# Optimization experiments

Hardware: AMD Instinct MI355X
Metric: run time of the kernel (lower is better)

The kernel has to match this reference:

```python
import jax, jax.numpy as jnp
import numpy as np

B, T, IN, H, OUT = 128, 1024, 17, 512, 17


def setup_inputs() -> dict:
    key = jax.random.key(0)
    ks = jax.random.split(key, 11)
    s_in = 1.0 / np.sqrt(H)
    return {
        "x": jax.random.normal(ks[0], (B, T, IN), dtype=jnp.float32),
        "wih0": jax.random.normal(ks[1], (4 * H, IN), dtype=jnp.float32) * s_in,
        "whh0": jax.random.normal(ks[2], (4 * H, H), dtype=jnp.float32) * s_in,
        "bih0": jax.random.normal(ks[3], (4 * H,), dtype=jnp.float32) * s_in,
        "bhh0": jax.random.normal(ks[4], (4 * H,), dtype=jnp.float32) * s_in,
        "wih1": jax.random.normal(ks[5], (4 * H, H), dtype=jnp.float32) * s_in,
        "whh1": jax.random.normal(ks[6], (4 * H, H), dtype=jnp.float32) * s_in,
        "bih1": jax.random.normal(ks[7], (4 * H,), dtype=jnp.float32) * s_in,
        "bhh1": jax.random.normal(ks[8], (4 * H,), dtype=jnp.float32) * s_in,
        "lin_w": jax.random.normal(ks[9], (OUT, H), dtype=jnp.float32) * s_in,
        "lin_b": jax.random.normal(ks[10], (OUT,), dtype=jnp.float32) * s_in,
    }


def _lstm_layer(x, wih, whh, bih, bhh):
    # x: [B, T, D]; gate order i, f, g, o (torch.nn.LSTMCell convention)
    b, _, _ = x.shape
    h = whh.shape[1]
    # Precompute input projection for all timesteps: [B, T, 4H]
    proj = jnp.einsum("btd,gd->btg", x, wih) + bih

    def step(carry, p_t):
        h_t, c_t = carry
        gates = p_t + h_t @ whh.T + bhh  # [B, 4H]
        i, f, g, o = jnp.split(gates, 4, axis=1)
        i = jax.nn.sigmoid(i)
        f = jax.nn.sigmoid(f)
        o = jax.nn.sigmoid(o)
        g = jnp.tanh(g)
        c_t = f * c_t + i * g
        h_t = o * jnp.tanh(c_t)
        return (h_t, c_t), h_t

    h0 = jnp.zeros((b, h), x.dtype)
    c0 = jnp.zeros((b, h), x.dtype)
    _, ys = jax.lax.scan(step, (h0, c0), jnp.swapaxes(proj, 0, 1))  # ys: [T, B, H]
    return jnp.swapaxes(ys, 0, 1)  # [B, T, H]


def reference(x, wih0, whh0, bih0, bhh0, wih1, whh1, bih1, bhh1, lin_w, lin_b):
    y = _lstm_layer(x, wih0, whh0, bih0, bhh0)
    y = _lstm_layer(y, wih1, whh1, bih1, bhh1)
    h_last = y[:, -1, :]  # [B, H]
    return h_last @ lin_w.T + lin_b  # [B, OUT]
```

## Files before the change

### kernel.cpp

```cpp
#include <hip/hip_runtime.h>
#include <cstddef>
#include <cstdint>

typedef unsigned long long ull;
typedef unsigned short u16;
typedef __attribute__((ext_vector_type(8))) short s8v;
typedef __attribute__((ext_vector_type(4))) float f4v;

#define GROUPS 8
#define WPG    32
#define BG     16
#define JS     16
#define TPB    256
#define NT     1024
#define HDIM   512
#define INDIM  17
#define OUTDIM 17
#define BTOT   128
#define RING_D 4

#define AT_LD(p)   __hip_atomic_load((p), __ATOMIC_RELAXED, __HIP_MEMORY_SCOPE_AGENT)
#define AT_ST(p,v) __hip_atomic_store((p), (v), __ATOMIC_RELAXED, __HIP_MEMORY_SCOPE_AGENT)

#define FLAGS_INTS (256 * 16)
#define RING_OFF   ((size_t)FLAGS_INTS * 4)
#define RING_ELEMS ((size_t)RING_D * GROUPS * 2 * BG * HDIM)
#define H1_OFF     (RING_OFF + RING_ELEMS * 2)
#define H1_ELEMS   ((size_t)2 * GROUPS * 2 * BG * HDIM)
#define WS_NEEDED  (H1_OFF + H1_ELEMS * 2)

#define RIDX(sl, gr, pl, b, j) \
  (((((size_t)(sl) * GROUPS + (gr)) * 2 + (pl)) * BG + (b)) * HDIM + (j))
#define H1IDX(pp, gr, pl, b, j) \
  (((((size_t)(pp) * GROUPS + (gr)) * 2 + (pl)) * BG + (b)) * HDIM + (j))

__device__ __forceinline__ u16 f2bf(float f) {
  unsigned int u = __float_as_uint(f);
  u += 0x7FFFu + ((u >> 16) & 1u);
  return (u16)(u >> 16);
}
__device__ __forceinline__ float bf2f(u16 h) {
  return __uint_as_float(((unsigned int)h) << 16);
}
__device__ __forceinline__ float sigm(float x) { return 1.f / (1.f + __expf(-x)); }
__device__ __forceinline__ float tanh_f(float x) { return 2.f / (1.f + __expf(-2.f * x)) - 1.f; }

#define MFMA(a, b, c) __builtin_amdgcn_mfma_f32_16x16x32_bf16((a), (b), (c), 0, 0, 0)

__global__ __launch_bounds__(TPB, 1) void lstm_fused(
    const float* __restrict__ x,
    const float* __restrict__ wih0, const float* __restrict__ whh0,
    const float* __restrict__ bih0, const float* __restrict__ bhh0,
    const float* __restrict__ wih1, const float* __restrict__ whh1,
    const float* __restrict__ bih1, const float* __restrict__ bhh1,
    u16* __restrict__ ring,
    u16* __restrict__ h1b,
    int* __restrict__ flags)
{
  const int bid  = blockIdx.x;
  const int gr   = bid & 7;
  const int wg   = bid >> 3;
  const int j0   = wg * JS;
  const int tid  = threadIdx.x;
  const int wave = tid >> 6;
  const int lane = tid & 63;
  const int n    = lane & 15;
  const int q    = lane >> 4;
  const int k0   = q * 8;

  __shared__ char smem[65536];
  char* b0h = smem;
  char* b0l = smem + 16384;
  char* b1h = smem + 32768;
  char* b1l = smem + 49152;
  float* ldsg = (float*)smem;

  const int row = wave * HDIM + j0 + n;
  s8v w0x_h, w0x_l;
  {
    const float* wr = wih0 + (size_t)row * INDIM;
#pragma unroll
    for (int j = 0; j < 8; ++j) {
      int k = k0 + j;
      float v = (k < INDIM) ? wr[k] : 0.f;
      u16 hi = f2bf(v);
      w0x_h[j] = (short)hi;
      w0x_l[j] = (short)f2bf(v - bf2f(hi));
    }
  }
  s8v w0h_h[16], w0h_l[16];
  {
    const float* wr = whh0 + (size_t)row * HDIM;
#pragma unroll
    for (int kt = 0; kt < 16; ++kt)
#pragma unroll
      for (int j = 0; j < 8; ++j) {
        float v = wr[kt * 32 + k0 + j];
        u16 hi = f2bf(v);
        w0h_h[kt][j] = (short)hi;
        w0h_l[kt][j] = (short)f2bf(v - bf2f(hi));
      }
  }
  s8v w1x_h[16];
  {
    const float* wr = wih1 + (size_t)row * HDIM;
#pragma unroll
    for (int kt = 0; kt < 16; ++kt)
#pragma unroll
      for (int j = 0; j < 8; ++j)
        w1x_h[kt][j] = (short)f2bf(wr[kt * 32 + k0 + j]);
  }
  s8v w1h_h[16], w1h_l[16];
  {
    const float* wr = whh1 + (size_t)row * HDIM;
#pragma unroll
    for (int kt = 0; kt < 16; ++kt)
#pragma unroll
      for (int j = 0; j < 8; ++j) {
        float v = wr[kt * 32 + k0 + j];
        u16 hi = f2bf(v);
        w1h_h[kt][j] = (short)hi;
        w1h_l[kt][j] = (short)f2bf(v - bf2f(hi));
      }
  }
  const float b0v = bih0[row] + bhh0[row];
  const float b1v = bih1[row] + bhh1[row];

  float c0 = 0.f, c1 = 0.f;
  const int b_l = tid >> 4, j_l = tid & 15, jg = j0 + j_l;

  AT_ST(&ring[RIDX(0, gr, 0, b_l, jg)], (u16)0);
  AT_ST(&ring[RIDX(0, gr, 1, b_l, jg)], (u16)0);
  AT_ST(&h1b[H1IDX(0, gr, 0, b_l, jg)], (u16)0);
  AT_ST(&h1b[H1IDX(0, gr, 1, b_l, jg)], (u16)0);
  __syncthreads();
  if (tid == 0) AT_ST(&flags[bid * 16], 1);

  for (int s = 1; s <= NT + 1; ++s) {
    const bool doL0 = (s <= NT);
    const bool doL1 = (s >= 2);

    f4v a0 = {b0v, b0v, b0v, b0v};
    if (doL0) {
      const int t = s - 1;
      const float* xr = x + ((size_t)(gr * BG + n) * NT + t) * INDIM;
      s8v axh, axl;
#pragma unroll
      for (int j = 0; j < 8; ++j) {
        int k = k0 + j;
        float v = (k < INDIM) ? xr[k] : 0.f;
        u16 hi = f2bf(v);
        axh[j] = (short)hi;
        axl[j] = (short)f2bf(v - bf2f(hi));
      }
      a0 = MFMA(axh, w0x_h, a0);
      a0 = MFMA(axl, w0x_h, a0);
      a0 = MFMA(axh, w0x_l, a0);
    }

    if (tid < WPG) {
      const int* fp = &flags[(tid * 8 + gr) * 16];
      while (AT_LD(fp) < s) __builtin_amdgcn_s_sleep(1);
    }
    __syncthreads();

    {
      const int sl  = (s - 1) & (RING_D - 1);
      const int pp1 = s & 1;
      const ull* g0h = (const ull*)(ring + RIDX(sl, gr, 0, 0, 0));
      const ull* g0l = (const ull*)(ring + RIDX(sl, gr, 1, 0, 0));
      const ull* g1h = (const ull*)(h1b + H1IDX(pp1, gr, 0, 0, 0));
      const ull* g1l = (const ull*)(h1b + H1IDX(pp1, gr, 1, 0, 0));
      ull v0h[8], v0l[8], v1h[8], v1l[8];
#pragma unroll
      for (int r = 0; r < 8; ++r) {
        int c = r * 256 + tid;
        v0h[r] = AT_LD(g0h + c);
        v0l[r] = AT_LD(g0l + c);
        v1h[r] = AT_LD(g1h + c);
        v1l[r] = AT_LD(g1l + c);
      }
#pragma unroll
      for (int r = 0; r < 8; ++r) {
        int c = r * 256 + tid;
        int b = c >> 7, k4 = c & 127;
        int off = b * 1024 + ((k4 * 8) ^ ((b & 7) * 16));
        *(ull*)(b0h + off) = v0h[r];
        *(ull*)(b0l + off) = v0l[r];
        *(ull*)(b1h + off) = v1h[r];
        *(ull*)(b1l + off) = v1l[r];
      }
    }
    __syncthreads();

    f4v z = {0.f, 0.f, 0.f, 0.f};
    f4v cA1 = z, cA2 = z, cB0 = {b1v, b1v, b1v, b1v}, cB1 = z;
#pragma unroll
    for (int kt = 0; kt < 16; ++kt) {
      int off = n * 1024 + ((kt * 64 + q * 16) ^ ((n & 7) * 16));
      s8v ah = *(const s8v*)(b0h + off);
      s8v al = *(const s8v*)(b0l + off);
      a0  = MFMA(ah, w0h_h[kt], a0);
      cA1 = MFMA(al, w0h_h[kt], cA1);
      cA2 = MFMA(ah, w0h_l[kt], cA2);
      cB0 = MFMA(ah, w1x_h[kt], cB0);
      cB1 = MFMA(al, w1x_h[kt], cB1);
    }
    f4v cC0 = z, cC1 = z, cC2 = z;
#pragma unroll
    for (int kt = 0; kt < 16; ++kt) {
      int off = n * 1024 + ((kt * 64 + q * 16) ^ ((n & 7) * 16));
      s8v ah = *(const s8v*)(b1h + off);
      s8v al = *(const s8v*)(b1l + off);
      cC0 = MFMA(ah, w1h_h[kt], cC0);
      cC1 = MFMA(al, w1h_h[kt], cC1);
      cC2 = MFMA(ah, w1h_l[kt], cC2);
    }
    __syncthreads();

    if (doL0) {
      f4v g = a0 + cA1 + cA2;
#pragma unroll
      for (int r = 0; r < 4; ++r) ldsg[wave * 256 + (q * 4 + r) * 16 + n] = g[r];
    }
    if (doL1) {
      f4v g = cB0 + cB1 + cC0 + cC1 + cC2;
#pragma unroll
      for (int r = 0; r < 4; ++r) ldsg[(4 + wave) * 256 + (q * 4 + r) * 16 + n] = g[r];
    }
    __syncthreads();

    if (doL0) {
      float pi = ldsg[0 * 256 + tid], pf = ldsg[1 * 256 + tid];
      float pg = ldsg[2 * 256 + tid], po = ldsg[3 * 256 + tid];
      float ig = sigm(pi), fg = sigm(pf), og = sigm(po), gg = tanh_f(pg);
      c0 = fg * c0 + ig * gg;
      float h = og * tanh_f(c0);
      u16 hh = f2bf(h), hl = f2bf(h - bf2f(hh));
      int sl = s & (RING_D - 1);
      AT_ST(&ring[RIDX(sl, gr, 0, b_l, jg)], hh);
      AT_ST(&ring[RIDX(sl, gr, 1, b_l, jg)], hl);
    }
    if (doL1) {
      float pi = ldsg[4 * 256 + tid], pf = ldsg[5 * 256 + tid];
      float pg = ldsg[6 * 256 + tid], po = ldsg[7 * 256 + tid];
      float ig = sigm(pi), fg = sigm(pf), og = sigm(po), gg = tanh_f(pg);
      c1 = fg * c1 + ig * gg;
      float h = og * tanh_f(c1);
      u16 hh = f2bf(h), hl = f2bf(h - bf2f(hh));
      int pw = (s - 1) & 1;
      AT_ST(&h1b[H1IDX(pw, gr, 0, b_l, jg)], hh);
      AT_ST(&h1b[H1IDX(pw, gr, 1, b_l, jg)], hl);
    }
    __syncthreads();
    if (doL0 && tid == 0) AT_ST(&flags[bid * 16], s + 1);
  }
}

__global__ void final_linear(const u16* __restrict__ h1b,
                             const float* __restrict__ lin_w,
                             const float* __restrict__ lin_b,
                             float* __restrict__ out) {
  int b = blockIdx.x, o = threadIdx.x;
  int gr = b >> 4, b_l = b & 15;
  if (o < OUTDIM) {
    float acc = lin_b[o];
    const u16* ph = h1b + H1IDX(0, gr, 0, b_l, 0);
    const u16* pl = h1b + H1IDX(0, gr, 1, b_l, 0);
    for (int j = 0; j < HDIM; ++j) {
      float h = bf2f(ph[j]) + bf2f(pl[j]);
      acc += h * lin_w[(size_t)o * HDIM + j];
    }
    out[b * OUTDIM + o] = acc;
  }
}

__global__ void init_flags(int* __restrict__ flags) {
  int i = blockIdx.x * TPB + threadIdx.x;
  if (i < FLAGS_INTS) flags[i] = 0;
}

__global__ void sentinel_kernel(float* __restrict__ out, int nv) {
  int i = blockIdx.x * TPB + threadIdx.x;
  if (i < nv) out[i] = 1e30f;
}

extern "C" void kernel_launch(void* const* d_in, const int* in_sizes, int n_in,
                              void* d_out, int out_size, void* d_ws, size_t ws_size,
                              hipStream_t stream) {
  const float* x     = (const float*)d_in[0];
  const float* wih0  = (const float*)d_in[1];
  const float* whh0  = (const float*)d_in[2];
  const float* bih0  = (const float*)d_in[3];
  const float* bhh0  = (const float*)d_in[4];
  const float* wih1  = (const float*)d_in[5];
  const float* whh1  = (const float*)d_in[6];
  const float* bih1  = (const float*)d_in[7];
  const float* bhh1  = (const float*)d_in[8];
  const float* lin_w = (const float*)d_in[9];
  const float* lin_b = (const float*)d_in[10];
  float* out = (float*)d_out;
  char* ws = (char*)d_ws;

  if (ws_size < WS_NEEDED) {
    sentinel_kernel<<<(out_size + TPB - 1) / TPB, TPB, 0, stream>>>(out, out_size);
    return;
  }

  int* flags = (int*)ws;
  u16* ring  = (u16*)(ws + RING_OFF);
  u16* h1b   = (u16*)(ws + H1_OFF);

  init_flags<<<(FLAGS_INTS + TPB - 1) / TPB, TPB, 0, stream>>>(flags);
  lstm_fused<<<256, TPB, 0, stream>>>(x, wih0, whh0, bih0, bhh0,
                                      wih1, whh1, bih1, bhh1, ring, h1b, flags);
  final_linear<<<BTOT, 64, 0, stream>>>(h1b, lin_w, lin_b, out);
}
```

Baseline: 5.472 ms.

## Split K across waves and load hidden state directly into MFMA registers

The work split inside each block changes. Before, each wave handled one gate over the full K=512. Now each wave handles all four gates over a 128-wide K slice, and the partial sums are reduced through a swizzled LDS buffer. The hidden-state operands are loaded straight from global memory into MFMA registers, which removes the LDS staging copy and one barrier per step. In exchange, each step adds a cross-wave reduction, and each wave now issues redundant global loads of its own K slice.

```diff
diff --git a/kernel.cpp b/kernel.cpp
--- a/kernel.cpp
+++ b/kernel.cpp
@@ -46,6 +46,13 @@
 __device__ __forceinline__ float tanh_f(float x) { return 2.f / (1.f + __expf(-2.f * x)) - 1.f; }
 
 #define MFMA(a, b, c) __builtin_amdgcn_mfma_f32_16x16x32_bf16((a), (b), (c), 0, 0, 0)
+
+__device__ __forceinline__ s8v ld16(const ull* p) {
+  union { ull q[2]; s8v v; } u;
+  u.q[0] = AT_LD(p);
+  u.q[1] = AT_LD(p + 1);
+  return u.v;
+}
 
 __global__ __launch_bounds__(TPB, 1) void lstm_fused(
     const float* __restrict__ x,
@@ -67,18 +74,13 @@
   const int n    = lane & 15;
   const int q    = lane >> 4;
   const int k0   = q * 8;
-
-  __shared__ char smem[65536];
-  char* b0h = smem;
-  char* b0l = smem + 16384;
-  char* b1h = smem + 32768;
-  char* b1l = smem + 49152;
-  float* ldsg = (float*)smem;
-
-  const int row = wave * HDIM + j0 + n;
+  const int kw   = wave * 128;
+
+  __shared__ float red[4 * 8 * 16 * 16];
+
   s8v w0x_h, w0x_l;
   {
-    const float* wr = wih0 + (size_t)row * INDIM;
+    const float* wr = wih0 + (size_t)(wave * HDIM + j0 + n) * INDIM;
 #pragma unroll
     for (int j = 0; j < 8; ++j) {
       int k = k0 + j;
@@ -88,46 +90,37 @@
       w0x_l[j] = (short)f2bf(v - bf2f(hi));
     }
   }
-  s8v w0h_h[16], w0h_l[16];
-  {
-    const float* wr = whh0 + (size_t)row * HDIM;
-#pragma unroll
-    for (int kt = 0; kt < 16; ++kt)
+  s8v w0hh[4][4], w0hl[4][4], w1xh[4][4], w1hh[4][4], w1hl[4][4];
+#pragma unroll
+  for (int g = 0; g < 4; ++g) {
+    const size_t row = (size_t)(g * HDIM + j0 + n);
+    const float* p0 = whh0 + row * HDIM;
+    const float* p1 = wih1 + row * HDIM;
+    const float* p2 = whh1 + row * HDIM;
+#pragma unroll
+    for (int kt = 0; kt < 4; ++kt) {
 #pragma unroll
       for (int j = 0; j < 8; ++j) {
-        float v = wr[kt * 32 + k0 + j];
-        u16 hi = f2bf(v);
-        w0h_h[kt][j] = (short)hi;
-        w0h_l[kt][j] = (short)f2bf(v - bf2f(hi));
-      }
-  }
-  s8v w1x_h[16];
-  {
-    const float* wr = wih1 + (size_t)row * HDIM;
-#pragma unroll
-    for (int kt = 0; kt < 16; ++kt)
-#pragma unroll
-      for (int j = 0; j < 8; ++j)
-        w1x_h[kt][j] = (short)f2bf(wr[kt * 32 + k0 + j]);
-  }
-  s8v w1h_h[16], w1h_l[16];
-  {
-    const float* wr = whh1 + (size_t)row * HDIM;
-#pragma unroll
-    for (int kt = 0; kt < 16; ++kt)
-#pragma unroll
-      for (int j = 0; j < 8; ++j) {
-        float v = wr[kt * 32 + k0 + j];
-        u16 hi = f2bf(v);
-        w1h_h[kt][j] = (short)hi;
-        w1h_l[kt][j] = (short)f2bf(v - bf2f(hi));
-      }
-  }
-  const float b0v = bih0[row] + bhh0[row];
-  const float b1v = bih1[row] + bhh1[row];
+        int k = kw + kt * 32 + k0 + j;
+        float v0 = p0[k], v2 = p2[k];
+        u16 h0q = f2bf(v0), h2q = f2bf(v2);
+        w0hh[g][kt][j] = (short)h0q;
+        w0hl[g][kt][j] = (short)f2bf(v0 - bf2f(h0q));
+        w1xh[g][kt][j] = (short)f2bf(p1[k]);
+        w1hh[g][kt][j] = (short)h2q;
+        w1hl[g][kt][j] = (short)f2bf(v2 - bf2f(h2q));
+      }
+    }
+  }
+  const int b_l = tid >> 4, j_l = tid & 15, jg = j0 + j_l;
+  float bL0[4], bL1[4];
+#pragma unroll
+  for (int g = 0; g < 4; ++g) {
+    bL0[g] = bih0[g * HDIM + jg] + bhh0[g * HDIM + jg];
+    bL1[g] = bih1[g * HDIM + jg] + bhh1[g * HDIM + jg];
+  }
 
   float c0 = 0.f, c1 = 0.f;
-  const int b_l = tid >> 4, j_l = tid & 15, jg = j0 + j_l;
 
   AT_ST(&ring[RIDX(0, gr, 0, b_l, jg)], (u16)0);
   AT_ST(&ring[RIDX(0, gr, 1, b_l, jg)], (u16)0);
@@ -136,11 +129,13 @@
   __syncthreads();
   if (tid == 0) AT_ST(&flags[bid * 16], 1);
 
+  const f4v z = {0.f, 0.f, 0.f, 0.f};
+
   for (int s = 1; s <= NT + 1; ++s) {
     const bool doL0 = (s <= NT);
     const bool doL1 = (s >= 2);
 
-    f4v a0 = {b0v, b0v, b0v, b0v};
+    f4v xacc = z;
     if (doL0) {
       const int t = s - 1;
       const float* xr = x + ((size_t)(gr * BG + n) * NT + t) * INDIM;
@@ -153,9 +148,9 @@
         axh[j] = (short)hi;
         axl[j] = (short)f2bf(v - bf2f(hi));
       }
-      a0 = MFMA(axh, w0x_h, a0);
-      a0 = MFMA(axl, w0x_h, a0);
-      a0 = MFMA(axh, w0x_l, a0);
+      xacc = MFMA(axh, w0x_h, xacc);
+      xacc = MFMA(axl, w0x_h, xacc);
+      xacc = MFMA(axh, w0x_l, xacc);
     }
 
     if (tid < WPG) {
@@ -164,87 +159,90 @@
     }
     __syncthreads();
 
-    {
-      const int sl  = (s - 1) & (RING_D - 1);
-      const int pp1 = s & 1;
-      const ull* g0h = (const ull*)(ring + RIDX(sl, gr, 0, 0, 0));
-      const ull* g0l = (const ull*)(ring + RIDX(sl, gr, 1, 0, 0));
-      const ull* g1h = (const ull*)(h1b + H1IDX(pp1, gr, 0, 0, 0));
-      const ull* g1l = (const ull*)(h1b + H1IDX(pp1, gr, 1, 0, 0));
-      ull v0h[8], v0l[8], v1h[8], v1l[8];
-#pragma unroll
-      for (int r = 0; r < 8; ++r) {
-        int c = r * 256 + tid;
-        v0h[r] = AT_LD(g0h + c);
-        v0l[r] = AT_LD(g0l + c);
-        v1h[r] = AT_LD(g1h + c);
-        v1l[r] = AT_LD(g1l + c);
-      }
-#pragma unroll
-      for (int r = 0; r < 8; ++r) {
-        int c = r * 256 + tid;
-        int b = c >> 7, k4 = c & 127;
-        int off = b * 1024 + ((k4 * 8) ^ ((b & 7) * 16));
-        *(ull*)(b0h + off) = v0h[r];
-        *(ull*)(b0l + off) = v0l[r];
-        *(ull*)(b1h + off) = v1h[r];
-        *(ull*)(b1l + off) = v1l[r];
-      }
+    const int sl  = (s - 1) & (RING_D - 1);
+    const int pp1 = s & 1;
+    const size_t loff = (size_t)n * HDIM + kw + k0;
+    const ull* r0h = (const ull*)(ring + RIDX(sl, gr, 0, 0, 0) + loff);
+    const ull* r0l = (const ull*)(ring + RIDX(sl, gr, 1, 0, 0) + loff);
+    const ull* r1h = (const ull*)(h1b + H1IDX(pp1, gr, 0, 0, 0) + loff);
+    const ull* r1l = (const ull*)(h1b + H1IDX(pp1, gr, 1, 0, 0) + loff);
+    s8v a0h[4], a0l[4], a1h[4], a1l[4];
+#pragma unroll
+    for (int kt = 0; kt < 4; ++kt) {
+      a0h[kt] = ld16(r0h + kt * 8);
+      a0l[kt] = ld16(r0l + kt * 8);
+    }
+#pragma unroll
+    for (int kt = 0; kt < 4; ++kt) {
+      a1h[kt] = ld16(r1h + kt * 8);
+      a1l[kt] = ld16(r1l + kt * 8);
+    }
+
+    f4v accL0[4] = {z, z, z, z}, accL1[4] = {z, z, z, z};
+#pragma unroll
+    for (int kt = 0; kt < 4; ++kt)
+#pragma unroll
+      for (int g = 0; g < 4; ++g) {
+        accL0[g] = MFMA(a0h[kt], w0hh[g][kt], accL0[g]);
+        accL0[g] = MFMA(a0l[kt], w0hh[g][kt], accL0[g]);
+        accL0[g] = MFMA(a0h[kt], w0hl[g][kt], accL0[g]);
+        accL1[g] = MFMA(a0h[kt], w1xh[g][kt], accL1[g]);
+        accL1[g] = MFMA(a0l[kt], w1xh[g][kt], accL1[g]);
+      }
+#pragma unroll
+    for (int kt = 0; kt < 4; ++kt)
+#pragma unroll
+      for (int g = 0; g < 4; ++g) {
+        accL1[g] = MFMA(a1h[kt], w1hh[g][kt], accL1[g]);
+        accL1[g] = MFMA(a1l[kt], w1hh[g][kt], accL1[g]);
+        accL1[g] = MFMA(a1h[kt], w1hl[g][kt], accL1[g]);
+      }
+    accL0[wave] += xacc;
+
+#pragma unroll
+    for (int lg = 0; lg < 8; ++lg) {
+      const f4v a = (lg < 4) ? accL0[lg] : accL1[lg - 4];
+      int base = ((wave * 8 + lg) * 16 + n) * 16;
+      int idx = (base + ((q * 4) ^ ((n & 3) << 2))) ^ ((n & 4) << 2);
+      *(f4v*)&red[idx] = a;
     }
     __syncthreads();
 
-    f4v z = {0.f, 0.f, 0.f, 0.f};
-    f4v cA1 = z, cA2 = z, cB0 = {b1v, b1v, b1v, b1v}, cB1 = z;
-#pragma unroll
-    for (int kt = 0; kt < 16; ++kt) {
-      int off = n * 1024 + ((kt * 64 + q * 16) ^ ((n & 7) * 16));
-      s8v ah = *(const s8v*)(b0h + off);
-      s8v al = *(const s8v*)(b0l + off);
-      a0  = MFMA(ah, w0h_h[kt], a0);
-      cA1 = MFMA(al, w0h_h[kt], cA1);
-      cA2 = MFMA(ah, w0h_l[kt], cA2);
-      cB0 = MFMA(ah, w1x_h[kt], cB0);
-      cB1 = MFMA(al, w1x_h[kt], cB1);
-    }
-    f4v cC0 = z, cC1 = z, cC2 = z;
-#pragma unroll
-    for (int kt = 0; kt < 16; ++kt) {
-      int off = n * 1024 + ((kt * 64 + q * 16) ^ ((n & 7) * 16));
-      s8v ah = *(const s8v*)(b1h + off);
-      s8v al = *(const s8v*)(b1l + off);
-      cC0 = MFMA(ah, w1h_h[kt], cC0);
-      cC1 = MFMA(al, w1h_h[kt], cC1);
-      cC2 = MFMA(ah, w1h_l[kt], cC2);
-    }
-    __syncthreads();
-
     if (doL0) {
-      f4v g = a0 + cA1 + cA2;
-#pragma unroll
-      for (int r = 0; r < 4; ++r) ldsg[wave * 256 + (q * 4 + r) * 16 + n] = g[r];
-    }
-    if (doL1) {
-      f4v g = cB0 + cB1 + cC0 + cC1 + cC2;
-#pragma unroll
-      for (int r = 0; r < 4; ++r) ldsg[(4 + wave) * 256 + (q * 4 + r) * 16 + n] = g[r];
-    }
-    __syncthreads();
-
-    if (doL0) {
-      float pi = ldsg[0 * 256 + tid], pf = ldsg[1 * 256 + tid];
-      float pg = ldsg[2 * 256 + tid], po = ldsg[3 * 256 + tid];
-      float ig = sigm(pi), fg = sigm(pf), og = sigm(po), gg = tanh_f(pg);
+      float p[4];
+#pragma unroll
+      for (int g = 0; g < 4; ++g) {
+        float t = bL0[g];
+#pragma unroll
+        for (int w = 0; w < 4; ++w) {
+          int base = ((w * 8 + g) * 16 + j_l) * 16;
+          int idx = (base + (b_l ^ ((j_l & 3) << 2))) ^ ((j_l & 4) << 2);
+          t += red[idx];
+        }
+        p[g] = t;
+      }
+      float ig = sigm(p[0]), fg = sigm(p[1]), og = sigm(p[3]), gg = tanh_f(p[2]);
       c0 = fg * c0 + ig * gg;
       float h = og * tanh_f(c0);
       u16 hh = f2bf(h), hl = f2bf(h - bf2f(hh));
-      int sl = s & (RING_D - 1);
-      AT_ST(&ring[RIDX(sl, gr, 0, b_l, jg)], hh);
-      AT_ST(&ring[RIDX(sl, gr, 1, b_l, jg)], hl);
+      int so = s & (RING_D - 1);
+      AT_ST(&ring[RIDX(so, gr, 0, b_l, jg)], hh);
+      AT_ST(&ring[RIDX(so, gr, 1, b_l, jg)], hl);
     }
     if (doL1) {
-      float pi = ldsg[4 * 256 + tid], pf = ldsg[5 * 256 + tid];
-      float pg = ldsg[6 * 256 + tid], po = ldsg[7 * 256 + tid];
-      float ig = sigm(pi), fg = sigm(pf), og = sigm(po), gg = tanh_f(pg);
+      float p[4];
+#pragma unroll
+      for (int g = 0; g < 4; ++g) {
+        float t = bL1[g];
+#pragma unroll
+        for (int w = 0; w < 4; ++w) {
+          int base = ((w * 8 + (4 + g)) * 16 + j_l) * 16;
+          int idx = (base + (b_l ^ ((j_l & 3) << 2))) ^ ((j_l & 4) << 2);
+          t += red[idx];
+        }
+        p[g] = t;
+      }
+      float ig = sigm(p[0]), fg = sigm(p[1]), og = sigm(p[3]), gg = tanh_f(p[2]);
       c1 = fg * c1 + ig * gg;
       float h = og * tanh_f(c1);
       u16 hh = f2bf(h), hl = f2bf(h - bf2f(hh));
```

Measured after the change: 7.967 ms. 45.6% more time.
